# Optimization experiments

Hardware: AMD Instinct MI355X
Metric: run time of the kernel (lower is better)

The kernel has to match this reference:

```python
import math
import jax, jax.numpy as jnp
import numpy as np

NUM_TOKENS = 8192
MODEL_DIM = 1024
NUM_EXPERTS = 64
CAPACITY_FACTOR = 1.0
MIN_CAPACITY = 8
SHIFT_PRIORITY = 0.5
LOAD_BALANCE_W = 0.01


def setup_inputs() -> dict:
    key = jax.random.key(0)
    k1, k2 = jax.random.split(key)
    x = jax.random.normal(k1, (NUM_TOKENS, MODEL_DIM), dtype=jnp.float32)
    # torch.nn.Linear(model_dim, num_experts, bias=False).weight -> [E, D]
    wg_weight = jax.random.normal(k2, (NUM_EXPERTS, MODEL_DIM), dtype=jnp.float32) * 0.02
    return {"x": x, "wg_weight": wg_weight}


def reference(x, wg_weight):
    S = x.shape[0]
    E = wg_weight.shape[0]
    # gate projection (fp32, as in DeepSpeed gating)
    logits = jnp.einsum('sd,ed->se', x, wg_weight)  # [S, E]
    gates = jax.nn.softmax(logits, axis=1)
    original_gates = gates

    # _capacity: ceil(S/E * capacity_factor), clamped to min_capacity (static)
    capacity = max(int(math.ceil(S / E * CAPACITY_FACTOR)), MIN_CAPACITY)

    indices1_s = jnp.argmax(gates, axis=1)                      # [S]
    mask1 = jax.nn.one_hot(indices1_s, E, dtype=jnp.int32)      # [S, E]
    exp_counts = jnp.sum(mask1, axis=0)                         # [E]

    # AuxLoss: GShard load-balance loss, zloss/entropy weights are 0
    me = jnp.mean(gates, axis=0)
    ce = jnp.mean(mask1.astype(gates.dtype), axis=0)
    l_aux = jnp.sum(me * ce) * E * LOAD_BALANCE_W

    # shifted-priority routing: sort tokens by -max_gate, roll, positional cumsum
    importance_scores = -jnp.max(gates, axis=1)                 # [S]
    sort_indices = jnp.argsort(importance_scores)               # [S]
    shift_num = int(S * SHIFT_PRIORITY)                         # static
    sort_indices = jnp.roll(sort_indices, shift_num)
    recover_indices = jnp.argsort(sort_indices)
    sorted_mask1 = mask1[sort_indices]                          # [S, E]
    sorted_cumsum1 = (jnp.cumsum(sorted_mask1, axis=0) - 1) * sorted_mask1
    locations1 = sorted_cumsum1[recover_indices]                # [S, E]

    # capacity dropping
    mask1 = mask1 * (locations1 < capacity).astype(jnp.int32)
    locations1_s = jnp.sum(locations1 * mask1, axis=1)          # [S]

    gates_masked = original_gates * mask1.astype(gates.dtype)   # [S, E]
    locations1_sc = jax.nn.one_hot(locations1_s, capacity, dtype=gates.dtype)  # [S, C]
    combine_weights = jnp.einsum('se,sc->sec', gates_masked, locations1_sc)    # [S, E, C]
    dispatch_mask = combine_weights.astype(bool)

    unrouted_token_rate = 1.0 - jnp.mean(jnp.any(dispatch_mask, axis=(-1, -2)).astype(jnp.float32))
    return l_aux, combine_weights, dispatch_mask, exp_counts, unrouted_token_rate
```

## Files before the change

### kernel.cpp

```cpp
#include <hip/hip_runtime.h>
#include <stdint.h>

#define S_TOK   8192
#define MODEL_D 1024
#define N_EXP   64
#define CAP     128
#define SHIFT   4096
#define SLAB    (N_EXP * CAP)
#define CDSIZE  ((size_t)S_TOK * SLAB)
#define OUT_FILL4 33554448

#define GEMM_BLOCKS 512
#define TPB         16


#define OFF_EXPERT   0
#define OFF_GATE     32768
#define OFF_KEY      65536
#define OFF_KEY2     98304
#define OFF_MEPART   131072
#define OFF_HIST     262144
#define OFF_WGT      393216

__device__ __forceinline__ unsigned f2key(float f) {
    unsigned b = __float_as_uint(f);
    return (b & 0x80000000u) ? ~b : (b | 0x80000000u);
}

__global__ __launch_bounds__(256) void k0_repack(const float* __restrict__ wg,
                                                 float* __restrict__ wgT4) {
    int id0 = blockIdx.x * 256 + threadIdx.x;
#pragma unroll
    for (int i = 0; i < 4; ++i) {
        int id = id0 + i * 16384;
        int e = id >> 10;
        int d = id & 1023;
        wgT4[((d >> 2) * 64 + e) * 4 + (d & 3)] = wg[id];
    }
}

__global__ __launch_bounds__(256) void k1_fill_gemm(
    const float* __restrict__ x, const float* __restrict__ wgT4,
    float* __restrict__ out,
    int* __restrict__ expert_id, float* __restrict__ gate1,
    unsigned* __restrict__ keys, float* __restrict__ me_part,
    int* __restrict__ hist_part)
{
    const int b = blockIdx.x;
    if (b >= GEMM_BLOCKS) {
        const float4 z = make_float4(0.f, 0.f, 0.f, 0.f);
        float4* out4 = (float4*)out;
        size_t i = (size_t)(b - GEMM_BLOCKS) * 256 + threadIdx.x;
        for (; i < OUT_FILL4; i += (size_t)8192 * 256) out4[i] = z;
        return;
    }

    __shared__ float xs[TPB][256];
    __shared__ float lg[TPB][65];
    __shared__ float mrow[TPB], zrow[TPB];
    __shared__ int   exrow[TPB];
    __shared__ int   hist[64];
    __shared__ float mep[4][64];

    const int tid  = threadIdx.x;
    const int lane = tid & 63;
    const int wv   = tid >> 6;
    const int tok0 = b * TPB;

    const float4* xg  = (const float4*)x;
    const float4* wg4 = (const float4*)wgT4;

    float acc[4] = {0.f, 0.f, 0.f, 0.f};

    for (int chunk = 0; chunk < 4; ++chunk) {
        __syncthreads();
#pragma unroll
        for (int i = 0; i < 4; ++i) {
            int linear = tid + 256 * i;
            int t  = linear >> 6;
            int c4 = linear & 63;
            ((float4*)xs)[t * 64 + c4] = xg[(size_t)(tok0 + t) * 256 + chunk * 64 + c4];
        }
        __syncthreads();

#pragma unroll 4
        for (int dd = 0; dd < 256; dd += 4) {
            int d = chunk * 256 + dd;
            float4 w = wg4[(d >> 2) * 64 + lane];
#pragma unroll
            for (int t = 0; t < 4; ++t) {
                float4 xv = *(const float4*)&xs[wv * 4 + t][dd];
                acc[t] = fmaf(xv.x, w.x, acc[t]);
                acc[t] = fmaf(xv.y, w.y, acc[t]);
                acc[t] = fmaf(xv.z, w.z, acc[t]);
                acc[t] = fmaf(xv.w, w.w, acc[t]);
            }
        }
    }
#pragma unroll
    for (int t = 0; t < 4; ++t) lg[wv * 4 + t][lane] = acc[t];
    __syncthreads();

    if (tid < 64) hist[tid] = 0;
    if (tid < TPB) {
        const int t = tid;
        float m = lg[t][0]; int am = 0;
        for (int e = 1; e < 64; ++e) {
            float v = lg[t][e];
            if (v > m) { m = v; am = e; }
        }
        float z = 0.f;
        for (int e = 0; e < 64; ++e) z += expf(lg[t][e] - m);
        float rz = 1.0f / z;
        mrow[t] = m; zrow[t] = rz; exrow[t] = am;
        int sG = tok0 + t;
        expert_id[sG] = am;
        gate1[sG] = rz;
        keys[sG] = f2key(-rz);
    }
    __syncthreads();

    if (tid < TPB) atomicAdd(&hist[exrow[tid]], 1);
    {
        const int e = tid & 63, tg = tid >> 6;
        float p = 0.f;
        for (int t = tg; t < TPB; t += 4) p += expf(lg[t][e] - mrow[t]) * zrow[t];
        mep[tg][e] = p;
    }
    __syncthreads();

    if (tid < 64) {
        me_part[b * 64 + tid] = mep[0][tid] + mep[1][tid] + mep[2][tid] + mep[3][tid];
        hist_part[b * 64 + tid] = hist[tid];
    }
}

__global__ __launch_bounds__(256) void k2_rank_scalars(
    const unsigned* __restrict__ keys, const int* __restrict__ expert_id,
    const float* __restrict__ me_part, const int* __restrict__ hist_part,
    unsigned* __restrict__ key2, float* __restrict__ out)
{
    const int tid = threadIdx.x;
    if (blockIdx.x == 256) {
        __shared__ float msum[4][64];
        __shared__ int   hsum[4][64];
        __shared__ float contrib[64];
        __shared__ int   keep[64];
        const int e = tid & 63, qt = tid >> 6;
        float ms = 0.f; int hs = 0;
        for (int p = qt * 128; p < qt * 128 + 128; ++p) {
            ms += me_part[p * 64 + e];
            hs += hist_part[p * 64 + e];
        }
        msum[qt][e] = ms; hsum[qt][e] = hs;
        __syncthreads();
        if (tid < 64) {
            float m = msum[0][tid] + msum[1][tid] + msum[2][tid] + msum[3][tid];
            int   h = hsum[0][tid] + hsum[1][tid] + hsum[2][tid] + hsum[3][tid];
            out[1 + 2 * CDSIZE + tid] = (float)h;
            contrib[tid] = (m * (1.0f / S_TOK)) * ((float)h * (1.0f / S_TOK));
            keep[tid] = (h < CAP) ? h : CAP;
        }
        __syncthreads();
        if (tid == 0) {
            float sum = 0.f; int kept = 0;
            for (int i = 0; i < 64; ++i) { sum += contrib[i]; kept += keep[i]; }
            out[0] = sum * (float)N_EXP * 0.01f;
            out[1 + 2 * CDSIZE + 64] = (float)(S_TOK - kept) * (1.0f / S_TOK);
        }
        return;
    }

    __shared__ uint4 k4[2048];
    const uint4* kg = (const uint4*)keys;
    for (int i = tid; i < 2048; i += 256) k4[i] = kg[i];
    __syncthreads();

    const int sl = tid >> 3, part = tid & 7;
    const int sG = blockIdx.x * 32 + sl;
    const unsigned myk = ((const unsigned*)k4)[sG];
    int cnt = 0;
    const int qbase = part * 256;
    for (int q = 0; q < 256; ++q) {
        int qq = (q + part) & 255;
        uint4 v = k4[qbase + qq];
        int j = (qbase + qq) * 4;
        cnt += (v.x < myk) || (v.x == myk && (j + 0) < sG);
        cnt += (v.y < myk) || (v.y == myk && (j + 1) < sG);
        cnt += (v.z < myk) || (v.z == myk && (j + 2) < sG);
        cnt += (v.w < myk) || (v.w == myk && (j + 3) < sG);
    }
    cnt += __shfl_down(cnt, 4);
    cnt += __shfl_down(cnt, 2);
    cnt += __shfl_down(cnt, 1);
    if (part == 0) {
        int pos = (cnt + SHIFT) & (S_TOK - 1);
        key2[sG] = ((unsigned)expert_id[sG] << 13) | (unsigned)pos;
    }
}

__global__ __launch_bounds__(256) void k3_loc_scatter(const unsigned* __restrict__ key2,
                                                      const float* __restrict__ gate1,
                                                      float* __restrict__ out)
{
    __shared__ uint4 k4[2048];
    const int tid = threadIdx.x;
    const uint4* kg = (const uint4*)key2;
    for (int i = tid; i < 2048; i += 256) k4[i] = kg[i];
    __syncthreads();

    const int sl = tid >> 3, part = tid & 7;
    const int sG = blockIdx.x * 32 + sl;
    const unsigned myk = ((const unsigned*)k4)[sG];
    const unsigned lo = myk & ~8191u;
    int cnt = 0;
    const int qbase = part * 256;
    for (int q = 0; q < 256; ++q) {
        int qq = (q + part) & 255;
        uint4 v = k4[qbase + qq];
        cnt += (v.x >= lo) && (v.x < myk);
        cnt += (v.y >= lo) && (v.y < myk);
        cnt += (v.z >= lo) && (v.z < myk);
        cnt += (v.w >= lo) && (v.w < myk);
    }
    cnt += __shfl_down(cnt, 4);
    cnt += __shfl_down(cnt, 2);
    cnt += __shfl_down(cnt, 1);
    if (part == 0 && cnt < CAP) {
        unsigned e = myk >> 13;
        size_t idx = 1 + (size_t)sG * SLAB + (size_t)e * CAP + (unsigned)cnt;
        out[idx] = gate1[sG];
        out[idx + CDSIZE] = 1.0f;
    }
}

extern "C" void kernel_launch(void* const* d_in, const int* in_sizes, int n_in,
                              void* d_out, int out_size, void* d_ws, size_t ws_size,
                              hipStream_t stream) {
    (void)in_sizes; (void)n_in; (void)out_size; (void)ws_size;
    const float* x  = (const float*)d_in[0];
    const float* wg = (const float*)d_in[1];
    float* out = (float*)d_out;
    char* ws = (char*)d_ws;

    int*      expert_id = (int*)(ws + OFF_EXPERT);
    float*    gate1     = (float*)(ws + OFF_GATE);
    unsigned* keys      = (unsigned*)(ws + OFF_KEY);
    unsigned* key2      = (unsigned*)(ws + OFF_KEY2);
    float*    me_part   = (float*)(ws + OFF_MEPART);
    int*      hist_part = (int*)(ws + OFF_HIST);
    float*    wgT4      = (float*)(ws + OFF_WGT);

    hipLaunchKernelGGL(k0_repack,       dim3(64),                dim3(256), 0, stream, wg, wgT4);
    hipLaunchKernelGGL(k1_fill_gemm,    dim3(GEMM_BLOCKS + 8192), dim3(256), 0, stream,
                       x, wgT4, out, expert_id, gate1, keys, me_part, hist_part);
    hipLaunchKernelGGL(k2_rank_scalars, dim3(257),               dim3(256), 0, stream,
                       keys, expert_id, me_part, hist_part, key2, out);
    hipLaunchKernelGGL(k3_loc_scatter,  dim3(256),               dim3(256), 0, stream,
                       key2, gate1, out);
}
```

Before: 713.1 us.

## Split output zero-fill across GEMM and rank kernels with nontemporal stores

The large zero-fill of the combine/dispatch output was done entirely inside the GEMM kernel. It is now split in half: the first half stays with the GEMM blocks and the second half moves into the rank kernel, so it can overlap with the O(S²) rank computation. The fill uses unrolled, fixed-stride nontemporal vector stores instead of a grid-stride loop, to reduce cache pollution. The scalar aux-loss and count block moves into the final scatter kernel, which still runs after the fill has completed.

```diff
diff --git a/kernel.cpp b/kernel.cpp
--- a/kernel.cpp
+++ b/kernel.cpp
@@ -9,9 +9,13 @@
 #define SLAB    (N_EXP * CAP)
 #define CDSIZE  ((size_t)S_TOK * SLAB)
 #define OUT_FILL4 33554448
+#define FILL_SPLIT4  16777216
+#define FILL_STRIDE4 2097152
 
 #define GEMM_BLOCKS 512
 #define TPB         16
+
+typedef float fx4 __attribute__((ext_vector_type(4)));
 
 
 #define OFF_EXPERT   0
@@ -48,10 +52,13 @@
 {
     const int b = blockIdx.x;
     if (b >= GEMM_BLOCKS) {
-        const float4 z = make_float4(0.f, 0.f, 0.f, 0.f);
-        float4* out4 = (float4*)out;
-        size_t i = (size_t)(b - GEMM_BLOCKS) * 256 + threadIdx.x;
-        for (; i < OUT_FILL4; i += (size_t)8192 * 256) out4[i] = z;
+        const fx4 z = (fx4)(0.f);
+        fx4* out4 = (fx4*)out;
+        size_t base = (size_t)(b - GEMM_BLOCKS) * 256 + threadIdx.x;
+#pragma unroll
+        for (int k = 0; k < 8; ++k) {
+            __builtin_nontemporal_store(z, &out4[base + (size_t)k * FILL_STRIDE4]);
+        }
         return;
     }
 
@@ -135,10 +142,56 @@
     }
 }
 
-__global__ __launch_bounds__(256) void k2_rank_scalars(
+__global__ __launch_bounds__(256) void k2_rank_fill(
     const unsigned* __restrict__ keys, const int* __restrict__ expert_id,
+    unsigned* __restrict__ key2, float* __restrict__ out)
+{
+    const int tid = threadIdx.x;
+    const int b = blockIdx.x;
+    if (b >= 256) {
+        const fx4 z = (fx4)(0.f);
+        fx4* out4 = (fx4*)out;
+        size_t base = (size_t)FILL_SPLIT4 + (size_t)(b - 256) * 256 + tid;
+#pragma unroll
+        for (int k = 0; k < 9; ++k) {
+            size_t i = base + (size_t)k * FILL_STRIDE4;
+            if (i < OUT_FILL4) __builtin_nontemporal_store(z, &out4[i]);
+        }
+        return;
+    }
+
+    __shared__ uint4 k4[2048];
+    const uint4* kg = (const uint4*)keys;
+    for (int i = tid; i < 2048; i += 256) k4[i] = kg[i];
+    __syncthreads();
+
+    const int sl = tid >> 3, part = tid & 7;
+    const int sG = b * 32 + sl;
+    const unsigned myk = ((const unsigned*)k4)[sG];
+    int cnt = 0;
+    const int qbase = part * 256;
+    for (int q = 0; q < 256; ++q) {
+        int qq = (q + part) & 255;
+        uint4 v = k4[qbase + qq];
+        int j = (qbase + qq) * 4;
+        cnt += (v.x < myk) || (v.x == myk && (j + 0) < sG);
+        cnt += (v.y < myk) || (v.y == myk && (j + 1) < sG);
+        cnt += (v.z < myk) || (v.z == myk && (j + 2) < sG);
+        cnt += (v.w < myk) || (v.w == myk && (j + 3) < sG);
+    }
+    cnt += __shfl_down(cnt, 4);
+    cnt += __shfl_down(cnt, 2);
+    cnt += __shfl_down(cnt, 1);
+    if (part == 0) {
+        int pos = (cnt + SHIFT) & (S_TOK - 1);
+        key2[sG] = ((unsigned)expert_id[sG] << 13) | (unsigned)pos;
+    }
+}
+
+__global__ __launch_bounds__(256) void k3_loc_scatter_scalars(
+    const unsigned* __restrict__ key2, const float* __restrict__ gate1,
     const float* __restrict__ me_part, const int* __restrict__ hist_part,
-    unsigned* __restrict__ key2, float* __restrict__ out)
+    float* __restrict__ out)
 {
     const int tid = threadIdx.x;
     if (blockIdx.x == 256) {
@@ -172,39 +225,6 @@
     }
 
     __shared__ uint4 k4[2048];
-    const uint4* kg = (const uint4*)keys;
-    for (int i = tid; i < 2048; i += 256) k4[i] = kg[i];
-    __syncthreads();
-
-    const int sl = tid >> 3, part = tid & 7;
-    const int sG = blockIdx.x * 32 + sl;
-    const unsigned myk = ((const unsigned*)k4)[sG];
-    int cnt = 0;
-    const int qbase = part * 256;
-    for (int q = 0; q < 256; ++q) {
-        int qq = (q + part) & 255;
-        uint4 v = k4[qbase + qq];
-        int j = (qbase + qq) * 4;
-        cnt += (v.x < myk) || (v.x == myk && (j + 0) < sG);
-        cnt += (v.y < myk) || (v.y == myk && (j + 1) < sG);
-        cnt += (v.z < myk) || (v.z == myk && (j + 2) < sG);
-        cnt += (v.w < myk) || (v.w == myk && (j + 3) < sG);
-    }
-    cnt += __shfl_down(cnt, 4);
-    cnt += __shfl_down(cnt, 2);
-    cnt += __shfl_down(cnt, 1);
-    if (part == 0) {
-        int pos = (cnt + SHIFT) & (S_TOK - 1);
-        key2[sG] = ((unsigned)expert_id[sG] << 13) | (unsigned)pos;
-    }
-}
-
-__global__ __launch_bounds__(256) void k3_loc_scatter(const unsigned* __restrict__ key2,
-                                                      const float* __restrict__ gate1,
-                                                      float* __restrict__ out)
-{
-    __shared__ uint4 k4[2048];
-    const int tid = threadIdx.x;
     const uint4* kg = (const uint4*)key2;
     for (int i = tid; i < 2048; i += 256) k4[i] = kg[i];
     __syncthreads();
@@ -251,11 +271,11 @@
     int*      hist_part = (int*)(ws + OFF_HIST);
     float*    wgT4      = (float*)(ws + OFF_WGT);
 
-    hipLaunchKernelGGL(k0_repack,       dim3(64),                dim3(256), 0, stream, wg, wgT4);
-    hipLaunchKernelGGL(k1_fill_gemm,    dim3(GEMM_BLOCKS + 8192), dim3(256), 0, stream,
+    hipLaunchKernelGGL(k0_repack,             dim3(64),                 dim3(256), 0, stream, wg, wgT4);
+    hipLaunchKernelGGL(k1_fill_gemm,          dim3(GEMM_BLOCKS + 8192), dim3(256), 0, stream,
                        x, wgT4, out, expert_id, gate1, keys, me_part, hist_part);
-    hipLaunchKernelGGL(k2_rank_scalars, dim3(257),               dim3(256), 0, stream,
-                       keys, expert_id, me_part, hist_part, key2, out);
-    hipLaunchKernelGGL(k3_loc_scatter,  dim3(256),               dim3(256), 0, stream,
-                       key2, gate1, out);
-}
+    hipLaunchKernelGGL(k2_rank_fill,          dim3(256 + 8192),         dim3(256), 0, stream,
+                       keys, expert_id, key2, out);
+    hipLaunchKernelGGL(k3_loc_scatter_scalars, dim3(257),               dim3(256), 0, stream,
+                       key2, gate1, me_part, hist_part, out);
+}
```

Result: faster. 650.0 us (-8.8%).
